# Kernel tuning notes

Hardware: AMD Instinct MI355X
Metric: run time of the kernel (lower is better)

The kernel has to match this reference:

```python
import jax, jax.numpy as jnp
import numpy as np

TEMPERATURE = 0.1
EPS = 1e-8  # torch cosine_similarity eps
NEG_FILL = -9e15

def setup_inputs() -> dict:
    key = jax.random.key(0)
    stacked_batch = jax.random.normal(key, (8192, 128), dtype=jnp.float32)
    return {"stacked_batch": stacked_batch}

def reference(stacked_batch) -> jnp.ndarray:
    n = stacked_batch.shape[0]
    # cosine similarity = normalized GEMM (equivalent to torch broadcast form)
    norm = jnp.maximum(jnp.linalg.norm(stacked_batch, axis=-1, keepdims=True), EPS)
    z = stacked_batch / norm                      # [N, D]
    sim = jnp.matmul(z, z.T) / TEMPERATURE        # [N, N]
    # mask self-similarity on the diagonal
    idx = jnp.arange(n)
    sim = sim.at[idx, idx].set(NEG_FILL)
    # positive pair for row i is column (i + N/2) mod N
    pos_cols = (idx + n // 2) % n
    pos = sim[idx, pos_cols]                      # [N]
    loss = jax.scipy.special.logsumexp(sim, axis=-1) - pos
    return loss.mean()
```

## Files before the change

kernel.cpp:

```cpp
#include <hip/hip_runtime.h>
#include <hip/hip_bf16.h>

#define N 8192
#define D 128
#define HALF_N 4096
#define SQRT_SCALE_LOG2E 3.79828236f
#define LN2 0.693147180559945f

#define BLOCK_ROWS 256
#define COLS_PER_ITER 64
#define COL_SPLITS 32
#define COLS_PER_BLOCK (N / COL_SPLITS)
#define ITERS (COLS_PER_BLOCK / COLS_PER_ITER)

typedef short frag8 __attribute__((ext_vector_type(8)));
typedef float f32x4 __attribute__((ext_vector_type(4)));
typedef const __attribute__((address_space(1))) unsigned int* gbl_u32p;
typedef __attribute__((address_space(3))) unsigned int* lds_u32p;

#define OFF_POS    0
#define OFF_PSUMS  (N)
#define OFF_ACC    (N + COL_SPLITS * N)
#define OFF_Z_BYTES ((OFF_ACC + 64) * 4)

__device__ __forceinline__ unsigned short f2bf(float f) {
    unsigned int u = __float_as_uint(f);
    u += 0x7FFFu + ((u >> 16) & 1u);
    return (unsigned short)(u >> 16);
}

__global__ __launch_bounds__(256) void k_normalize(const float* __restrict__ x,
                                                   unsigned short* __restrict__ z,
                                                   float* __restrict__ acc0) {
    const int row  = blockIdx.x * 4 + (threadIdx.x >> 6);
    const int lane = threadIdx.x & 63;
    float2 v = ((const float2*)x)[row * 64 + lane];
    float s = v.x * v.x + v.y * v.y;
    #pragma unroll
    for (int m = 32; m >= 1; m >>= 1) s += __shfl_xor(s, m);
    float inv = SQRT_SCALE_LOG2E / fmaxf(sqrtf(s), 1e-8f);
    ushort2 o;
    o.x = f2bf(v.x * inv);
    o.y = f2bf(v.y * inv);
    ((ushort2*)z)[row * 64 + lane] = o;
    if (blockIdx.x == 0 && threadIdx.x == 0) acc0[0] = 0.0f;
}

__device__ __forceinline__ void stage_tile(const unsigned short* __restrict__ z,
                                           unsigned short* ldsbuf,
                                           int colbase, int wave,
                                           const int* stg_src) {
    const unsigned short* zc = z + (size_t)colbase * D;
    #pragma unroll
    for (int u = 0; u < 4; ++u) {
        __builtin_amdgcn_global_load_lds((gbl_u32p)(zc + stg_src[u]),
                                         (lds_u32p)(ldsbuf + (wave * 16 + u * 4) * D),
                                         16, 0, 0);
    }
}

__global__ __launch_bounds__(256, 2) void k_simloss(const unsigned short* __restrict__ z,
                                                    float* __restrict__ psums,
                                                    float* __restrict__ pos) {
    __shared__ unsigned short lds[2][COLS_PER_ITER * D];

    const int tid  = threadIdx.x;
    const int wave = tid >> 6;
    const int lane = tid & 63;
    const int l15  = lane & 15;
    const int quad = lane >> 4;
    const int l7   = l15 & 7;
    const int wrow = blockIdx.x * BLOCK_ROWS + wave * 64;
    const int colbase0 = blockIdx.y * COLS_PER_BLOCK;
    const int posbase  = (wrow + HALF_N) & (N - 1);

    int stg_src[4];
    #pragma unroll
    for (int u = 0; u < 4; ++u) {
        int r = wave * 16 + u * 4 + (lane >> 4);
        stg_src[u] = r * D + ((l15 ^ (r & 7)) << 3);
    }

    int boff[4];
    #pragma unroll
    for (int q = 0; q < 4; ++q)
        boff[q] = l15 * D + (((quad + 4 * q) ^ l7) << 3);

    frag8 a[4][4];
    #pragma unroll
    for (int s = 0; s < 4; ++s) {
        const uint4* p = (const uint4*)&z[(wrow + s * 16 + l15) * D + quad * 8];
        #pragma unroll
        for (int q = 0; q < 4; ++q) {
            uint4 t = p[q * 4];
            a[s][q] = *(frag8*)&t;
        }
    }

    float sums[4][4];
    #pragma unroll
    for (int s = 0; s < 4; ++s)
        #pragma unroll
        for (int r = 0; r < 4; ++r) sums[s][r] = 0.0f;

    stage_tile(z, &lds[0][0], colbase0, wave, stg_src);
    __syncthreads();

    #pragma unroll 1
    for (int it = 0; it < ITERS; ++it) {
        if (it + 1 < ITERS)
            stage_tile(z, &lds[(it + 1) & 1][0], colbase0 + (it + 1) * COLS_PER_ITER, wave, stg_src);

        const int colbase = colbase0 + it * COLS_PER_ITER;
        const bool isDiag = (colbase == wrow);
        const bool isPos  = (colbase == posbase);
        const unsigned short* lb = &lds[it & 1][0];

        #pragma unroll
        for (int c = 0; c < 4; ++c) {
            f32x4 acc[4];
            #pragma unroll
            for (int s = 0; s < 4; ++s) acc[s] = (f32x4){0.f, 0.f, 0.f, 0.f};
            #pragma unroll
            for (int q = 0; q < 4; ++q) {
                frag8 b = *(const frag8*)&lb[c * (16 * D) + boff[q]];
                #pragma unroll
                for (int s = 0; s < 4; ++s)
                    acc[s] = __builtin_amdgcn_mfma_f32_16x16x32_bf16(a[s][q], b, acc[s], 0, 0, 0);
            }
            if (isDiag | isPos) {
                #pragma unroll
                for (int s = 0; s < 4; ++s)
                    #pragma unroll
                    for (int r = 0; r < 4; ++r) {
                        float v = acc[s][r];
                        float e = __builtin_amdgcn_exp2f(v);
                        if (c == s) {
                            bool hit = (l15 == quad * 4 + r);
                            if (isDiag && hit) e = 0.0f;
                            if (isPos  && hit) pos[wrow + s * 16 + quad * 4 + r] = v * LN2;
                        }
                        sums[s][r] += e;
                    }
            } else {
                #pragma unroll
                for (int s = 0; s < 4; ++s)
                    #pragma unroll
                    for (int r = 0; r < 4; ++r)
                        sums[s][r] += __builtin_amdgcn_exp2f(acc[s][r]);
            }
        }
        __syncthreads();
    }

    #pragma unroll
    for (int s = 0; s < 4; ++s)
        #pragma unroll
        for (int r = 0; r < 4; ++r) {
            float v = sums[s][r];
            v += __shfl_xor(v, 1);
            v += __shfl_xor(v, 2);
            v += __shfl_xor(v, 4);
            v += __shfl_xor(v, 8);
            if (l15 == 0)
                psums[blockIdx.y * N + wrow + s * 16 + quad * 4 + r] = v;
        }
}

__global__ __launch_bounds__(1024) void k_rowloss(const float* __restrict__ psums,
                                                  const float* __restrict__ pos,
                                                  float* __restrict__ acc0) {
    const int row = blockIdx.x * 1024 + threadIdx.x;
    float t = 0.0f;
    #pragma unroll
    for (int s = 0; s < COL_SPLITS; ++s) t += psums[s * N + row];
    float loss = __logf(t) - pos[row];
    #pragma unroll
    for (int m = 32; m >= 1; m >>= 1) loss += __shfl_xor(loss, m);
    __shared__ float p[16];
    if ((threadIdx.x & 63) == 0) p[threadIdx.x >> 6] = loss;
    __syncthreads();
    if (threadIdx.x == 0) {
        float s = 0.0f;
        #pragma unroll
        for (int w = 0; w < 16; ++w) s += p[w];
        atomicAdd(acc0, s);
    }
}

__global__ void k_final(const float* __restrict__ acc0, float* __restrict__ out) {
    out[0] = acc0[0] * (1.0f / N);
}

extern "C" void kernel_launch(void* const* d_in, const int* in_sizes, int n_in,
                              void* d_out, int out_size, void* d_ws, size_t ws_size,
                              hipStream_t stream) {
    const float* x = (const float*)d_in[0];
    float* wsf   = (float*)d_ws;
    float* pos   = wsf + OFF_POS;
    float* psums = wsf + OFF_PSUMS;
    float* acc0  = wsf + OFF_ACC;
    unsigned short* z = (unsigned short*)((char*)d_ws + OFF_Z_BYTES);

    k_normalize<<<N / 4, 256, 0, stream>>>(x, z, acc0);
    dim3 g2(N / BLOCK_ROWS, COL_SPLITS);
    k_simloss<<<g2, 256, 0, stream>>>(z, psums, pos);
    k_rowloss<<<N / 1024, 1024, 0, stream>>>(psums, pos, acc0);
    k_final<<<1, 1, 0, stream>>>(acc0, (float*)d_out);
}
```

Measured before the change: 88.71 us.

## Exploit symmetry of similarity matrix, computing only upper-triangular tiles

After: 90.24 us. About the same (+1.7%).

```diff
diff --git a/kernel.cpp b/kernel.cpp
--- a/kernel.cpp
+++ b/kernel.cpp
@@ -9,8 +9,8 @@
 
 #define BLOCK_ROWS 256
 #define COLS_PER_ITER 64
-#define COL_SPLITS 32
-#define COLS_PER_BLOCK (N / COL_SPLITS)
+#define NCB 32
+#define COLS_PER_BLOCK 256
 #define ITERS (COLS_PER_BLOCK / COLS_PER_ITER)
 
 typedef short frag8 __attribute__((ext_vector_type(8)));
@@ -19,8 +19,9 @@
 typedef __attribute__((address_space(3))) unsigned int* lds_u32p;
 
 #define OFF_POS    0
-#define OFF_PSUMS  (N)
-#define OFF_ACC    (N + COL_SPLITS * N)
+#define OFF_PSR    (N)
+#define OFF_PSC    (N + NCB * N)
+#define OFF_ACC    (N + 2 * NCB * N)
 #define OFF_Z_BYTES ((OFF_ACC + 64) * 4)
 
 __device__ __forceinline__ unsigned short f2bf(float f) {
@@ -60,9 +61,15 @@
 }
 
 __global__ __launch_bounds__(256, 2) void k_simloss(const unsigned short* __restrict__ z,
-                                                    float* __restrict__ psums,
+                                                    float* __restrict__ psumsR,
+                                                    float* __restrict__ psumsC,
                                                     float* __restrict__ pos) {
+    const int bx = blockIdx.x;
+    const int by = blockIdx.y;
+    if (by < bx) return;
+
     __shared__ unsigned short lds[2][COLS_PER_ITER * D];
+    __shared__ float ldscol[4 * 256];
 
     const int tid  = threadIdx.x;
     const int wave = tid >> 6;
@@ -70,9 +77,10 @@
     const int l15  = lane & 15;
     const int quad = lane >> 4;
     const int l7   = l15 & 7;
-    const int wrow = blockIdx.x * BLOCK_ROWS + wave * 64;
-    const int colbase0 = blockIdx.y * COLS_PER_BLOCK;
+    const int wrow = bx * BLOCK_ROWS + wave * 64;
+    const int colbase0 = by * COLS_PER_BLOCK;
     const int posbase  = (wrow + HALF_N) & (N - 1);
+    const bool diagBlk = (bx == by);
 
     int stg_src[4];
     #pragma unroll
@@ -115,6 +123,8 @@
         const bool isDiag = (colbase == wrow);
         const bool isPos  = (colbase == posbase);
         const unsigned short* lb = &lds[it & 1][0];
+
+        float cs = 0.0f;
 
         #pragma unroll
         for (int c = 0; c < 4; ++c) {
@@ -128,6 +138,7 @@
                 for (int s = 0; s < 4; ++s)
                     acc[s] = __builtin_amdgcn_mfma_f32_16x16x32_bf16(a[s][q], b, acc[s], 0, 0, 0);
             }
+            float cc = 0.0f;
             if (isDiag | isPos) {
                 #pragma unroll
                 for (int s = 0; s < 4; ++s)
@@ -138,18 +149,32 @@
                         if (c == s) {
                             bool hit = (l15 == quad * 4 + r);
                             if (isDiag && hit) e = 0.0f;
-                            if (isPos  && hit) pos[wrow + s * 16 + quad * 4 + r] = v * LN2;
+                            if (isPos && hit) {
+                                int row = wrow + s * 16 + quad * 4 + r;
+                                float pv = v * LN2;
+                                pos[row] = pv;
+                                pos[row + HALF_N] = pv;
+                            }
                         }
                         sums[s][r] += e;
+                        cc += e;
                     }
             } else {
                 #pragma unroll
                 for (int s = 0; s < 4; ++s)
                     #pragma unroll
-                    for (int r = 0; r < 4; ++r)
-                        sums[s][r] += __builtin_amdgcn_exp2f(acc[s][r]);
+                    for (int r = 0; r < 4; ++r) {
+                        float e = __builtin_amdgcn_exp2f(acc[s][r]);
+                        sums[s][r] += e;
+                        cc += e;
+                    }
             }
+            cc += __shfl_xor(cc, 16);
+            cc += __shfl_xor(cc, 32);
+            if (quad == c) cs = cc;
         }
+        ldscol[wave * 256 + it * 64 + quad * 16 + l15] = cs;
+
         __syncthreads();
     }
 
@@ -163,29 +188,35 @@
             v += __shfl_xor(v, 4);
             v += __shfl_xor(v, 8);
             if (l15 == 0)
-                psums[blockIdx.y * N + wrow + s * 16 + quad * 4 + r] = v;
+                psumsR[by * N + wrow + s * 16 + quad * 4 + r] = v;
         }
-}
-
-__global__ __launch_bounds__(1024) void k_rowloss(const float* __restrict__ psums,
-                                                  const float* __restrict__ pos,
-                                                  float* __restrict__ acc0) {
-    const int row = blockIdx.x * 1024 + threadIdx.x;
+
+    if (!diagBlk) {
+        float v = ldscol[tid] + ldscol[256 + tid] + ldscol[512 + tid] + ldscol[768 + tid];
+        psumsC[bx * N + colbase0 + tid] = v;
+    }
+}
+
+__global__ __launch_bounds__(256) void k_rowloss(const float* __restrict__ psumsR,
+                                                 const float* __restrict__ psumsC,
+                                                 const float* __restrict__ pos,
+                                                 float* __restrict__ acc0) {
+    const int row = blockIdx.x * 256 + threadIdx.x;
+    const int R = row >> 8;
     float t = 0.0f;
     #pragma unroll
-    for (int s = 0; s < COL_SPLITS; ++s) t += psums[s * N + row];
+    for (int k = 0; k < NCB; ++k) {
+        const float* p = (k >= R) ? psumsR : psumsC;
+        t += p[k * N + row];
+    }
     float loss = __logf(t) - pos[row];
     #pragma unroll
     for (int m = 32; m >= 1; m >>= 1) loss += __shfl_xor(loss, m);
-    __shared__ float p[16];
-    if ((threadIdx.x & 63) == 0) p[threadIdx.x >> 6] = loss;
+    __shared__ float pp[4];
+    if ((threadIdx.x & 63) == 0) pp[threadIdx.x >> 6] = loss;
     __syncthreads();
-    if (threadIdx.x == 0) {
-        float s = 0.0f;
-        #pragma unroll
-        for (int w = 0; w < 16; ++w) s += p[w];
-        atomicAdd(acc0, s);
-    }
+    if (threadIdx.x == 0)
+        atomicAdd(acc0, pp[0] + pp[1] + pp[2] + pp[3]);
 }
 
 __global__ void k_final(const float* __restrict__ acc0, float* __restrict__ out) {
@@ -196,15 +227,16 @@
                               void* d_out, int out_size, void* d_ws, size_t ws_size,
                               hipStream_t stream) {
     const float* x = (const float*)d_in[0];
-    float* wsf   = (float*)d_ws;
-    float* pos   = wsf + OFF_POS;
-    float* psums = wsf + OFF_PSUMS;
-    float* acc0  = wsf + OFF_ACC;
+    float* wsf    = (float*)d_ws;
+    float* pos    = wsf + OFF_POS;
+    float* psumsR = wsf + OFF_PSR;
+    float* psumsC = wsf + OFF_PSC;
+    float* acc0   = wsf + OFF_ACC;
     unsigned short* z = (unsigned short*)((char*)d_ws + OFF_Z_BYTES);
 
     k_normalize<<<N / 4, 256, 0, stream>>>(x, z, acc0);
-    dim3 g2(N / BLOCK_ROWS, COL_SPLITS);
-    k_simloss<<<g2, 256, 0, stream>>>(z, psums, pos);
-    k_rowloss<<<N / 1024, 1024, 0, stream>>>(psums, pos, acc0);
+    dim3 g2(N / BLOCK_ROWS, NCB);
+    k_simloss<<<g2, 256, 0, stream>>>(z, psumsR, psumsC, pos);
+    k_rowloss<<<N / 256, 256, 0, stream>>>(psumsR, psumsC, pos, acc0);
     k_final<<<1, 1, 0, stream>>>(acc0, (float*)d_out);
 }
```
